# Kernel tuning notes

Hardware: AMD Instinct MI355X
Metric: run time of the kernel (lower is better)

The kernel has to match this reference:

```python
import jax, jax.numpy as jnp
import numpy as np

B, OBS, ACT_DIM, C, CTX, H = 128, 512, 7, 100, 128, 512
IN = OBS + 1 + CTX  # states + scalar action component + context = 641


def cont2disc(values, n):
    return jnp.clip(jnp.floor((values + 1.0) / 2.0 * n), 0, n - 1)


def setup_inputs() -> dict:
    key = jax.random.key(0)
    ks = jax.random.split(key, 10)
    def w(k, shape):
        return jax.random.normal(k, shape, dtype=jnp.float32) / np.sqrt(shape[-2])
    return {
        "observations": jax.random.normal(ks[0], (B, OBS), dtype=jnp.float32),
        "actions": jax.random.uniform(ks[1], (B, ACT_DIM), dtype=jnp.float32, minval=-1.0, maxval=1.0),
        # one MLP per action dim (weight_sharing=False): layers IN->H->H->CTX
        "W1": w(ks[2], (ACT_DIM, IN, H)),  "b1": jnp.zeros((ACT_DIM, H), jnp.float32),
        "W2": w(ks[3], (ACT_DIM, H, H)),   "b2": jnp.zeros((ACT_DIM, H), jnp.float32),
        "W3": w(ks[4], (ACT_DIM, H, CTX)), "b3": jnp.zeros((ACT_DIM, CTX), jnp.float32),
        # output_proj = MLP((1,)): single dense CTX->1, no activation
        "Wp": w(ks[5], (CTX, 1)), "bp": jnp.zeros((1,), jnp.float32),
        "compute_lse": 1,
    }


def reference(observations, actions, W1, b1, W2, b2, W3, b3, Wp, bp, compute_lse):
    n = observations.shape[0]
    acts = cont2disc(actions, C)  # [B, ACT_DIM], float component indices
    context = jnp.zeros((n, CTX), observations.dtype)
    comp = jnp.arange(C, dtype=observations.dtype)  # candidate components 0..C-1
    q = jnp.zeros((n, ACT_DIM * C), observations.dtype)

    for i in range(1, ACT_DIM):
        def mlp(x, i=i):  # hidden layers relu, final layer linear
            h = jax.nn.relu(x @ W1[i] + b1[i])
            h = jax.nn.relu(h @ W2[i] + b2[i])
            return h @ W3[i] + b3[i]

        # batched over all num_components candidate actions (replaces the per-j loop)
        xin = jnp.concatenate([
            jnp.broadcast_to(observations[:, None, :], (n, C, OBS)),
            jnp.broadcast_to(comp[None, :, None], (n, C, 1)),
            jnp.broadcast_to(context[:, None, :], (n, C, CTX)),
        ], axis=-1)  # [B, C, IN]
        curr_ctx = mlp(xin) + context[:, None, :]        # [B, C, CTX]
        qv = (curr_ctx @ Wp + bp)[..., 0]                # [B, C]
        q = q.at[:, (i - 1) * C : i * C].set(qv)          # which_qval ordering

        # advance context with the actual (discretized) action
        x = jnp.concatenate([observations, acts[:, i:i + 1], context], axis=-1)
        context = mlp(x) + context

    if compute_lse:
        return jax.scipy.special.logsumexp(q, axis=-1)    # [B]
    return context @ Wp + bp                              # [B, 1]
```

## Files before the change

### kernel.cpp

```cpp
#include <hip/hip_runtime.h>
#include <math.h>

#define BATCH 128
#define ACT 7
#define NC 100
#define CTXD 128
#define HID 512
#define QW 600

typedef __attribute__((ext_vector_type(8))) __bf16 bf16x8;
typedef __attribute__((ext_vector_type(4))) float f32x4;
typedef __attribute__((ext_vector_type(8))) unsigned short u16x8;
typedef __attribute__((ext_vector_type(4))) unsigned short u16x4;

__device__ __forceinline__ unsigned short f2bf(float f) {
    union { float f; unsigned int u; } v; v.f = f;
    unsigned int u = v.u;
    return (unsigned short)((u + 0x7fffu + ((u >> 16) & 1u)) >> 16);
}

__device__ __forceinline__ void async16(const void* g, void* l) {
    __builtin_amdgcn_global_load_lds(
        (const __attribute__((address_space(1))) unsigned int*)(uintptr_t)g,
        (__attribute__((address_space(3))) unsigned int*)(unsigned int)(uintptr_t)l,
        16, 0, 0);
}

__global__ void cvt_kernel(const float* __restrict__ obs, const float* __restrict__ W1,
                           const float* __restrict__ W2, const float* __restrict__ W3,
                           unsigned short* __restrict__ obs_bf, unsigned short* __restrict__ W1Cbf,
                           unsigned short* __restrict__ W2bf, unsigned short* __restrict__ W3bf) {
    const int e = (blockIdx.x * 256 + threadIdx.x) * 4;
    const float* src; unsigned short* dst;
    if (e < 65536)        { src = obs + e; dst = obs_bf + e; }
    else if (e < 458752)  { int f = e - 65536; int i = f >> 16; int rem = f & 65535;
                            src = W1 + (size_t)(i + 1) * 328192 + 513*512 + rem; dst = W1Cbf + f; }
    else if (e < 2031616) { int f = e - 458752; src = W2 + 262144 + f; dst = W2bf + f; }
    else                  { int f = e - 2031616; src = W3 + 65536 + f; dst = W3bf + f; }
    float4 v = *(const float4*)src;
    u16x4 o; o[0] = f2bf(v.x); o[1] = f2bf(v.y); o[2] = f2bf(v.z); o[3] = f2bf(v.w);
    *(u16x4*)dst = o;
}

__global__ void prep_transpose(const float* __restrict__ W1, const float* __restrict__ W2,
                               const float* __restrict__ W3,
                               unsigned short* __restrict__ W1AT, unsigned short* __restrict__ W2T,
                               unsigned short* __restrict__ W3T) {
    __shared__ float tile[32][33];
    const int z = blockIdx.z;
    const float* ip; unsigned short* op; int Cn;
    if (z < 6)       { ip = W1 + (size_t)(z + 1) * 328192; op = W1AT + (size_t)z * 262144; Cn = 512; }
    else if (z < 12) { int i = z - 6;  ip = W2 + (size_t)(i + 1) * 262144; op = W2T + (size_t)i * 262144; Cn = 512; }
    else             { int i = z - 12; ip = W3 + (size_t)(i + 1) * 65536;  op = W3T + (size_t)i * 65536;  Cn = 128;
                       if (blockIdx.y >= 4) return; }
    const int r0 = blockIdx.x * 32, c0 = blockIdx.y * 32;
    const int tx = threadIdx.x, ty = threadIdx.y;
    #pragma unroll
    for (int j = 0; j < 32; j += 8)
        tile[ty + j][tx] = ip[(size_t)(r0 + ty + j) * Cn + c0 + tx];
    __syncthreads();
    #pragma unroll
    for (int j = 0; j < 32; j += 8)
        op[(size_t)(c0 + ty + j) * 512 + r0 + tx] = f2bf(tile[tx][ty + j]);
}

__launch_bounds__(256)
__global__ void yobs_kernel(const unsigned short* __restrict__ A,
                            const unsigned short* __restrict__ BtAll,
                            const float* __restrict__ b1,
                            float* __restrict__ Yobs) {
    __shared__ unsigned short As[64*32];
    __shared__ unsigned short Bs[128*32];
    const int m0 = blockIdx.x * 64;
    const int n0 = blockIdx.y * 128;
    const int z  = blockIdx.z;
    const unsigned short* Bt = BtAll + (size_t)z * 262144;
    const int tid = threadIdx.x, lane = tid & 63, wave = tid >> 6;
    const int wm = wave >> 1, wn = wave & 1;
    const int srow = tid >> 2, skc = (tid & 3) * 8;
    const unsigned short* gA  = A  + (size_t)(m0 + srow) * HID + skc;
    const unsigned short* gB0 = Bt + (size_t)(n0 + srow) * HID + skc;
    const unsigned short* gB1 = gB0 + 64 * HID;
    f32x4 acc[2][4] = {};
    for (int k0 = 0; k0 < HID; k0 += 32) {
        async16(gA + k0, As + tid*8);
        async16(gB0 + k0, Bs + tid*8);
        async16(gB1 + k0, Bs + 2048 + tid*8);
        __syncthreads();
        const int q8 = (lane >> 4) * 8, l15 = lane & 15;
        bf16x8 af[2], bfr[4];
        #pragma unroll
        for (int mt = 0; mt < 2; ++mt)
            af[mt] = *(const bf16x8*)(As + (wm*32 + mt*16 + l15) * 32 + q8);
        #pragma unroll
        for (int nt = 0; nt < 4; ++nt)
            bfr[nt] = *(const bf16x8*)(Bs + (wn*64 + nt*16 + l15) * 32 + q8);
        #pragma unroll
        for (int mt = 0; mt < 2; ++mt)
            #pragma unroll
            for (int nt = 0; nt < 4; ++nt)
                acc[mt][nt] = __builtin_amdgcn_mfma_f32_16x16x32_bf16(af[mt], bfr[nt], acc[mt][nt], 0, 0, 0);
        __syncthreads();
    }
    const int colL = wn*64 + (lane & 15);
    #pragma unroll
    for (int nt = 0; nt < 4; ++nt) {
        const int col = n0 + colL + nt*16;
        const float bb = b1[(z + 1) * HID + col];
        #pragma unroll
        for (int mt = 0; mt < 2; ++mt)
            #pragma unroll
            for (int r = 0; r < 4; ++r) {
                const int row = m0 + wm*32 + mt*16 + (lane >> 4)*4 + r;
                Yobs[(size_t)z * 65536 + (size_t)row * HID + col] = acc[mt][nt][r] + bb;
            }
    }
}

__launch_bounds__(1024)
__global__ void chain_kernel(const float* __restrict__ Yobs, const float* __restrict__ W1,
                             const unsigned short* __restrict__ W1Cbf,
                             const unsigned short* __restrict__ W2bf,
                             const unsigned short* __restrict__ W3bf,
                             const float* __restrict__ b2, const float* __restrict__ b3,
                             const float* __restrict__ actions,
                             float* __restrict__ Y0all, float* __restrict__ CTXS) {
    const int b = blockIdx.x, t = threadIdx.x;
    __shared__ float ctx[128], h1[512], h2s[512];
    __shared__ float part[2048];
    const int pair = t & 255, kq = t >> 8;
    const int pair3 = t & 63, kq3 = t >> 6;
    if (t < 128) ctx[t] = 0.f;
    __syncthreads();
    for (int i = 1; i <= 6; ++i) {
        if (t < 128) CTXS[(size_t)(i-1)*16384 + b*128 + t] = ctx[t];
        const float a = actions[b*ACT + i];
        float fj = floorf((a + 1.0f) * 50.0f);
        fj = fminf(fmaxf(fj, 0.0f), 99.0f);
        {
            const unsigned int* wp1 = (const unsigned int*)(W1Cbf + (size_t)(i-1)*65536) + pair;
            float acc0 = 0.f, acc1 = 0.f;
            #pragma unroll 8
            for (int k = kq*32; k < kq*32 + 32; ++k) {
                unsigned int u = wp1[k*256];
                float c = ctx[k];
                acc0 = fmaf(c, __uint_as_float(u << 16), acc0);
                acc1 = fmaf(c, __uint_as_float(u & 0xffff0000u), acc1);
            }
            *(float2*)(&part[kq*512 + 2*pair]) = make_float2(acc0, acc1);
        }
        __syncthreads();
        if (t < 256) {
            const int n2 = 2*t;
            float2 p0 = *(const float2*)(&part[n2]);
            float2 p1 = *(const float2*)(&part[512 + n2]);
            float2 p2 = *(const float2*)(&part[1024 + n2]);
            float2 p3 = *(const float2*)(&part[1536 + n2]);
            float2 yo = *(const float2*)(Yobs + (size_t)(i-1)*65536 + b*512 + n2);
            float y0a = yo.x + p0.x + p1.x + p2.x + p3.x;
            float y0b = yo.y + p0.y + p1.y + p2.y + p3.y;
            *(float2*)(Y0all + (size_t)(i-1)*65536 + b*512 + n2) = make_float2(y0a, y0b);
            const float* w1a = W1 + (size_t)i*328192 + 262144;
            float2 wv = *(const float2*)(w1a + n2);
            h1[n2]   = fmaxf(fmaf(fj, wv.x, y0a), 0.f);
            h1[n2+1] = fmaxf(fmaf(fj, wv.y, y0b), 0.f);
        }
        __syncthreads();
        {
            const unsigned int* wp2 = (const unsigned int*)(W2bf + (size_t)(i-1)*262144) + pair;
            float acc0 = 0.f, acc1 = 0.f;
            #pragma unroll 8
            for (int k = kq*128; k < kq*128 + 128; ++k) {
                unsigned int u = wp2[k*256];
                float hv = h1[k];
                acc0 = fmaf(hv, __uint_as_float(u << 16), acc0);
                acc1 = fmaf(hv, __uint_as_float(u & 0xffff0000u), acc1);
            }
            *(float2*)(&part[kq*512 + 2*pair]) = make_float2(acc0, acc1);
        }
        __syncthreads();
        if (t < 256) {
            const int n2 = 2*t;
            float2 p0 = *(const float2*)(&part[n2]);
            float2 p1 = *(const float2*)(&part[512 + n2]);
            float2 p2 = *(const float2*)(&part[1024 + n2]);
            float2 p3 = *(const float2*)(&part[1536 + n2]);
            float2 bb = *(const float2*)(b2 + i*512 + n2);
            h2s[n2]   = fmaxf(p0.x + p1.x + p2.x + p3.x + bb.x, 0.f);
            h2s[n2+1] = fmaxf(p0.y + p1.y + p2.y + p3.y + bb.y, 0.f);
        }
        __syncthreads();
        {
            const unsigned int* wp3 = (const unsigned int*)(W3bf + (size_t)(i-1)*65536) + pair3;
            float acc0 = 0.f, acc1 = 0.f;
            #pragma unroll 8
            for (int k = kq3*32; k < kq3*32 + 32; ++k) {
                unsigned int u = wp3[k*64];
                float hv = h2s[k];
                acc0 = fmaf(hv, __uint_as_float(u << 16), acc0);
                acc1 = fmaf(hv, __uint_as_float(u & 0xffff0000u), acc1);
            }
            *(float2*)(&part[kq3*128 + 2*pair3]) = make_float2(acc0, acc1);
        }
        __syncthreads();
        if (t < 128) {
            float s = 0.f;
            #pragma unroll
            for (int qg = 0; qg < 16; ++qg) s += part[qg*128 + t];
            ctx[t] = s + b3[i*128 + t] + ctx[t];
        }
        __syncthreads();
    }
}

__launch_bounds__(256)
__global__ void h2all_kernel(const float* __restrict__ Y0all, const float* __restrict__ W1,
                             const unsigned short* __restrict__ W2T, const float* __restrict__ b2,
                             unsigned short* __restrict__ H2) {
    __shared__ unsigned short As[2][4096];
    __shared__ unsigned short Bs[2][4096];
    const int bx = blockIdx.x;
    const int z  = bx / 100;
    const int r0 = bx * 128;
    const int r2 = (bx % 100) * 128;
    const int n0 = blockIdx.y * 128;
    const int tid = threadIdx.x, lane = tid & 63, wave = tid >> 6;
    const int wm = wave >> 1, wn = wave & 1;
    const int srow = tid >> 2, skc = (tid & 3) * 8;
    const int l15 = lane & 15, q8 = (lane >> 4) * 8;
    const int rA = srow, kc = skc;
    const int rowg1 = r2 + rA, rowg2 = r2 + rA + 64;
    const float c1 = (float)(rowg1 % 100), c2 = (float)(rowg2 % 100);
    const float* y1p = Y0all + (size_t)z*65536 + (size_t)(rowg1/100)*512;
    const float* y2p = Y0all + (size_t)z*65536 + (size_t)(rowg2/100)*512;
    const float* w1a = W1 + (size_t)(z+1)*328192 + 262144;
    const unsigned short* gB0 = W2T + (size_t)z*262144 + (size_t)(n0 + srow)*512 + skc;
    const unsigned short* gB1 = gB0 + 64*512;
    f32x4 acc[4][4] = {};
    for (int k0 = 0; k0 < 512; k0 += 64) {
        #pragma unroll
        for (int h = 0; h < 2; ++h) {
            const int k = k0 + h*32 + kc;
            float4 wv0 = *(const float4*)(w1a + k);
            float4 wv1 = *(const float4*)(w1a + k + 4);
            float4 ya0 = *(const float4*)(y1p + k);
            float4 ya1 = *(const float4*)(y1p + k + 4);
            float4 yb0 = *(const float4*)(y2p + k);
            float4 yb1 = *(const float4*)(y2p + k + 4);
            u16x8 o1, o2;
            o1[0] = f2bf(fmaxf(fmaf(c1, wv0.x, ya0.x), 0.f));
            o1[1] = f2bf(fmaxf(fmaf(c1, wv0.y, ya0.y), 0.f));
            o1[2] = f2bf(fmaxf(fmaf(c1, wv0.z, ya0.z), 0.f));
            o1[3] = f2bf(fmaxf(fmaf(c1, wv0.w, ya0.w), 0.f));
            o1[4] = f2bf(fmaxf(fmaf(c1, wv1.x, ya1.x), 0.f));
            o1[5] = f2bf(fmaxf(fmaf(c1, wv1.y, ya1.y), 0.f));
            o1[6] = f2bf(fmaxf(fmaf(c1, wv1.z, ya1.z), 0.f));
            o1[7] = f2bf(fmaxf(fmaf(c1, wv1.w, ya1.w), 0.f));
            o2[0] = f2bf(fmaxf(fmaf(c2, wv0.x, yb0.x), 0.f));
            o2[1] = f2bf(fmaxf(fmaf(c2, wv0.y, yb0.y), 0.f));
            o2[2] = f2bf(fmaxf(fmaf(c2, wv0.z, yb0.z), 0.f));
            o2[3] = f2bf(fmaxf(fmaf(c2, wv0.w, yb0.w), 0.f));
            o2[4] = f2bf(fmaxf(fmaf(c2, wv1.x, yb1.x), 0.f));
            o2[5] = f2bf(fmaxf(fmaf(c2, wv1.y, yb1.y), 0.f));
            o2[6] = f2bf(fmaxf(fmaf(c2, wv1.z, yb1.z), 0.f));
            o2[7] = f2bf(fmaxf(fmaf(c2, wv1.w, yb1.w), 0.f));
            *(u16x8*)(&As[h][rA*32 + kc]) = o1;
            *(u16x8*)(&As[h][(rA + 64)*32 + kc]) = o2;
        }
        async16(gB0 + k0,      &Bs[0][tid*8]);
        async16(gB1 + k0,      &Bs[0][2048 + tid*8]);
        async16(gB0 + k0 + 32, &Bs[1][tid*8]);
        async16(gB1 + k0 + 32, &Bs[1][2048 + tid*8]);
        __syncthreads();
        #pragma unroll
        for (int h = 0; h < 2; ++h) {
            bf16x8 af[4], bfr[4];
            #pragma unroll
            for (int mt = 0; mt < 4; ++mt)
                af[mt] = *(const bf16x8*)(&As[h][(wm*64 + mt*16 + l15)*32 + q8]);
            #pragma unroll
            for (int nt = 0; nt < 4; ++nt)
                bfr[nt] = *(const bf16x8*)(&Bs[h][(wn*64 + nt*16 + l15)*32 + q8]);
            #pragma unroll
            for (int mt = 0; mt < 4; ++mt)
                #pragma unroll
                for (int nt = 0; nt < 4; ++nt)
                    acc[mt][nt] = __builtin_amdgcn_mfma_f32_16x16x32_bf16(af[mt], bfr[nt], acc[mt][nt], 0, 0, 0);
        }
        __syncthreads();
    }
    #pragma unroll
    for (int nt = 0; nt < 4; ++nt) {
        const int col = n0 + wn*64 + nt*16 + l15;
        const float bb = b2[(z+1)*512 + col];
        #pragma unroll
        for (int mt = 0; mt < 4; ++mt)
            #pragma unroll
            for (int r = 0; r < 4; ++r) {
                const int row = r0 + wm*64 + mt*16 + (lane >> 4)*4 + r;
                H2[(size_t)row * 512 + col] = f2bf(fmaxf(acc[mt][nt][r] + bb, 0.f));
            }
    }
}

__launch_bounds__(256)
__global__ void gemm3all_kernel(const unsigned short* __restrict__ H2,
                                const unsigned short* __restrict__ W3T,
                                const float* __restrict__ b3, const float* __restrict__ CTXS,
                                const float* __restrict__ Wp, const float* __restrict__ bp,
                                float* __restrict__ q) {
    __shared__ unsigned short As[2][1024];
    __shared__ unsigned short Bs[2][4096];
    __shared__ float CCs[32][132];
    __shared__ float qp[32][8];
    const int bx = blockIdx.x;
    const int z  = bx / 400;
    const int r0 = bx * 32;
    const int r2 = (bx % 400) * 32;
    const int tid = threadIdx.x, lane = tid & 63, wave = tid >> 6;
    const int wm = wave >> 1, wn = wave & 1;
    const int srow = tid >> 2, skc = (tid & 3) * 8;
    const int l15 = lane & 15, q8 = (lane >> 4) * 8;
    const unsigned short* gB0 = W3T + (size_t)z*65536 + (size_t)srow*512 + skc;
    const unsigned short* gB1 = gB0 + 64*512;
    const unsigned short* gA  = H2 + (size_t)(r0 + srow)*512 + skc;
    f32x4 acc[4] = {};
    for (int k0 = 0; k0 < 512; k0 += 64) {
        if (tid < 128) {
            async16(gA + k0,      &As[0][tid*8]);
            async16(gA + k0 + 32, &As[1][tid*8]);
        }
        async16(gB0 + k0,      &Bs[0][tid*8]);
        async16(gB1 + k0,      &Bs[0][2048 + tid*8]);
        async16(gB0 + k0 + 32, &Bs[1][tid*8]);
        async16(gB1 + k0 + 32, &Bs[1][2048 + tid*8]);
        __syncthreads();
        #pragma unroll
        for (int h = 0; h < 2; ++h) {
            bf16x8 af = *(const bf16x8*)(&As[h][(wm*16 + l15)*32 + q8]);
            #pragma unroll
            for (int nt = 0; nt < 4; ++nt) {
                bf16x8 bfr = *(const bf16x8*)(&Bs[h][(wn*64 + nt*16 + l15)*32 + q8]);
                acc[nt] = __builtin_amdgcn_mfma_f32_16x16x32_bf16(af, bfr, acc[nt], 0, 0, 0);
            }
        }
        __syncthreads();
    }
    #pragma unroll
    for (int nt = 0; nt < 4; ++nt) {
        const int col = wn*64 + nt*16 + l15;
        const float bb = b3[(z+1)*128 + col];
        #pragma unroll
        for (int r = 0; r < 4; ++r) {
            const int rowL = wm*16 + (lane >> 4)*4 + r;
            const int gb = (r2 + rowL) / 100;
            CCs[rowL][col] = acc[nt][r] + bb + CTXS[(size_t)z*16384 + gb*128 + col];
        }
    }
    __syncthreads();
    {
        const int rowL = tid >> 3, seg = tid & 7;
        float s = 0.f;
        #pragma unroll
        for (int j = 0; j < 16; ++j) s += CCs[rowL][seg*16 + j] * Wp[seg*16 + j];
        qp[rowL][seg] = s;
    }
    __syncthreads();
    if (tid < 32) {
        const int gr2 = r2 + tid;
        const int gb = gr2 / 100, gc = gr2 - gb * 100;
        float s = qp[tid][0] + qp[tid][1] + qp[tid][2] + qp[tid][3]
                + qp[tid][4] + qp[tid][5] + qp[tid][6] + qp[tid][7];
        q[gb * QW + z * 100 + gc] = s + bp[0];
    }
}

__global__ void lse_kernel(const float* __restrict__ q, float* __restrict__ out) {
    __shared__ float red[256];
    int b = blockIdx.x, t = threadIdx.x;
    float m = 0.0f;
    for (int k = t; k < QW; k += 256) m = fmaxf(m, q[b*QW + k]);
    red[t] = m; __syncthreads();
    for (int s = 128; s > 0; s >>= 1) { if (t < s) red[t] = fmaxf(red[t], red[t+s]); __syncthreads(); }
    m = red[0]; __syncthreads();
    float sum = 0.0f;
    for (int k = t; k < QW; k += 256) sum += expf(q[b*QW + k] - m);
    red[t] = sum; __syncthreads();
    for (int s = 128; s > 0; s >>= 1) { if (t < s) red[t] += red[t+s]; __syncthreads(); }
    if (t == 0) out[b] = logf(red[0] + 100.0f * expf(-m)) + m;
}

extern "C" void kernel_launch(void* const* d_in, const int* in_sizes, int n_in,
                              void* d_out, int out_size, void* d_ws, size_t ws_size,
                              hipStream_t stream) {
    const float* obs     = (const float*)d_in[0];
    const float* actions = (const float*)d_in[1];
    const float* W1      = (const float*)d_in[2];
    const float* b1      = (const float*)d_in[3];
    const float* W2      = (const float*)d_in[4];
    const float* b2      = (const float*)d_in[5];
    const float* W3      = (const float*)d_in[6];
    const float* b3      = (const float*)d_in[7];
    const float* Wp      = (const float*)d_in[8];
    const float* bp      = (const float*)d_in[9];
    float* out = (float*)d_out;
    float* ws  = (float*)d_ws;

    unsigned short* obs_bf = (unsigned short*)(ws);
    unsigned short* W1AT   = (unsigned short*)(ws + 32768);
    unsigned short* W2T    = (unsigned short*)(ws + 819200);
    unsigned short* W3T    = (unsigned short*)(ws + 1605632);
    unsigned short* W1Cbf  = (unsigned short*)(ws + 1802240);
    unsigned short* W2bf   = (unsigned short*)(ws + 1998848);
    unsigned short* W3bf   = (unsigned short*)(ws + 2785280);
    float* Yobs  = ws + 2981888;
    float* Y0all = ws + 3375104;
    float* CTXS  = ws + 3768320;
    float* q     = ws + 3866624;
    unsigned short* H2 = (unsigned short*)(ws + 3943424);

    cvt_kernel<<<2368, 256, 0, stream>>>(obs, W1, W2, W3, obs_bf, W1Cbf, W2bf, W3bf);
    prep_transpose<<<dim3(16,16,18), dim3(32,8), 0, stream>>>(W1, W2, W3, W1AT, W2T, W3T);
    yobs_kernel<<<dim3(2,4,6), 256, 0, stream>>>(obs_bf, W1AT, b1, Yobs);
    chain_kernel<<<BATCH, 1024, 0, stream>>>(Yobs, W1, W1Cbf, W2bf, W3bf, b2, b3, actions, Y0all, CTXS);
    h2all_kernel<<<dim3(600, 4), 256, 0, stream>>>(Y0all, W1, W2T, b2, H2);
    gemm3all_kernel<<<2400, 256, 0, stream>>>(H2, W3T, b3, CTXS, Wp, bp, q);
    lse_kernel<<<BATCH, 256, 0, stream>>>(q, out);
}
```

Before: 263.3 us.

## Retile layer-2 and layer-3 GEMMs to full-width N with 64-row blocks

The h2all GEMM now gives each block 64 rows and all 512 output columns, with a 32-wide K step. The fused ReLU/first-layer A tile is therefore computed once per row instead of once per 128-column slice, which removes the fourfold recomputation and the repeated Y0all reads. gemm3all moves from 32-row to 64-row tiles so each W3 tile load is reused across more rows, and the chain kernel's layer-2 loop gets a larger unroll. In exchange the per-thread accumulator count grows to 32 f32x4 vectors, which raises register pressure (launch bounds now ask for two blocks per CU). The K loop also does twice as many barrier steps with no double buffering.

Measured after the change: 269.4 us. 2.3% more time.

```diff
diff --git a/kernel.cpp b/kernel.cpp
--- a/kernel.cpp
+++ b/kernel.cpp
@@ -169,7 +169,7 @@
         {
             const unsigned int* wp2 = (const unsigned int*)(W2bf + (size_t)(i-1)*262144) + pair;
             float acc0 = 0.f, acc1 = 0.f;
-            #pragma unroll 8
+            #pragma unroll 16
             for (int k = kq*128; k < kq*128 + 128; ++k) {
                 unsigned int u = wp2[k*256];
                 float hv = h1[k];
@@ -213,91 +213,72 @@
     }
 }
 
-__launch_bounds__(256)
+__launch_bounds__(256, 2)
 __global__ void h2all_kernel(const float* __restrict__ Y0all, const float* __restrict__ W1,
                              const unsigned short* __restrict__ W2T, const float* __restrict__ b2,
                              unsigned short* __restrict__ H2) {
-    __shared__ unsigned short As[2][4096];
-    __shared__ unsigned short Bs[2][4096];
+    __shared__ unsigned short ASl[64*32];
+    __shared__ unsigned short BSl[512*32];
     const int bx = blockIdx.x;
-    const int z  = bx / 100;
-    const int r0 = bx * 128;
-    const int r2 = (bx % 100) * 128;
-    const int n0 = blockIdx.y * 128;
+    const int z  = bx / 200;
+    const int r0 = bx * 64;
+    const int r2 = (bx % 200) * 64;
     const int tid = threadIdx.x, lane = tid & 63, wave = tid >> 6;
-    const int wm = wave >> 1, wn = wave & 1;
-    const int srow = tid >> 2, skc = (tid & 3) * 8;
     const int l15 = lane & 15, q8 = (lane >> 4) * 8;
-    const int rA = srow, kc = skc;
-    const int rowg1 = r2 + rA, rowg2 = r2 + rA + 64;
-    const float c1 = (float)(rowg1 % 100), c2 = (float)(rowg2 % 100);
-    const float* y1p = Y0all + (size_t)z*65536 + (size_t)(rowg1/100)*512;
-    const float* y2p = Y0all + (size_t)z*65536 + (size_t)(rowg2/100)*512;
-    const float* w1a = W1 + (size_t)(z+1)*328192 + 262144;
-    const unsigned short* gB0 = W2T + (size_t)z*262144 + (size_t)(n0 + srow)*512 + skc;
-    const unsigned short* gB1 = gB0 + 64*512;
-    f32x4 acc[4][4] = {};
-    for (int k0 = 0; k0 < 512; k0 += 64) {
-        #pragma unroll
-        for (int h = 0; h < 2; ++h) {
-            const int k = k0 + h*32 + kc;
-            float4 wv0 = *(const float4*)(w1a + k);
-            float4 wv1 = *(const float4*)(w1a + k + 4);
-            float4 ya0 = *(const float4*)(y1p + k);
-            float4 ya1 = *(const float4*)(y1p + k + 4);
-            float4 yb0 = *(const float4*)(y2p + k);
-            float4 yb1 = *(const float4*)(y2p + k + 4);
-            u16x8 o1, o2;
-            o1[0] = f2bf(fmaxf(fmaf(c1, wv0.x, ya0.x), 0.f));
-            o1[1] = f2bf(fmaxf(fmaf(c1, wv0.y, ya0.y), 0.f));
-            o1[2] = f2bf(fmaxf(fmaf(c1, wv0.z, ya0.z), 0.f));
-            o1[3] = f2bf(fmaxf(fmaf(c1, wv0.w, ya0.w), 0.f));
-            o1[4] = f2bf(fmaxf(fmaf(c1, wv1.x, ya1.x), 0.f));
-            o1[5] = f2bf(fmaxf(fmaf(c1, wv1.y, ya1.y), 0.f));
-            o1[6] = f2bf(fmaxf(fmaf(c1, wv1.z, ya1.z), 0.f));
-            o1[7] = f2bf(fmaxf(fmaf(c1, wv1.w, ya1.w), 0.f));
-            o2[0] = f2bf(fmaxf(fmaf(c2, wv0.x, yb0.x), 0.f));
-            o2[1] = f2bf(fmaxf(fmaf(c2, wv0.y, yb0.y), 0.f));
-            o2[2] = f2bf(fmaxf(fmaf(c2, wv0.z, yb0.z), 0.f));
-            o2[3] = f2bf(fmaxf(fmaf(c2, wv0.w, yb0.w), 0.f));
-            o2[4] = f2bf(fmaxf(fmaf(c2, wv1.x, yb1.x), 0.f));
-            o2[5] = f2bf(fmaxf(fmaf(c2, wv1.y, yb1.y), 0.f));
-            o2[6] = f2bf(fmaxf(fmaf(c2, wv1.z, yb1.z), 0.f));
-            o2[7] = f2bf(fmaxf(fmaf(c2, wv1.w, yb1.w), 0.f));
-            *(u16x8*)(&As[h][rA*32 + kc]) = o1;
-            *(u16x8*)(&As[h][(rA + 64)*32 + kc]) = o2;
-        }
-        async16(gB0 + k0,      &Bs[0][tid*8]);
-        async16(gB1 + k0,      &Bs[0][2048 + tid*8]);
-        async16(gB0 + k0 + 32, &Bs[1][tid*8]);
-        async16(gB1 + k0 + 32, &Bs[1][2048 + tid*8]);
-        __syncthreads();
-        #pragma unroll
-        for (int h = 0; h < 2; ++h) {
-            bf16x8 af[4], bfr[4];
-            #pragma unroll
-            for (int mt = 0; mt < 4; ++mt)
-                af[mt] = *(const bf16x8*)(&As[h][(wm*64 + mt*16 + l15)*32 + q8]);
-            #pragma unroll
-            for (int nt = 0; nt < 4; ++nt)
-                bfr[nt] = *(const bf16x8*)(&Bs[h][(wn*64 + nt*16 + l15)*32 + q8]);
-            #pragma unroll
-            for (int mt = 0; mt < 4; ++mt)
-                #pragma unroll
-                for (int nt = 0; nt < 4; ++nt)
-                    acc[mt][nt] = __builtin_amdgcn_mfma_f32_16x16x32_bf16(af[mt], bfr[nt], acc[mt][nt], 0, 0, 0);
-        }
+    const int rA = tid >> 2, kc8 = (tid & 3) * 8;
+    const int growA = r2 + rA;
+    const float cA = (float)(growA % 100);
+    const float* yp  = Y0all + (size_t)z*65536 + (size_t)(growA/100)*512 + kc8;
+    const float* w1a = W1 + (size_t)(z+1)*328192 + 262144 + kc8;
+    const unsigned short* W2Tz = W2T + (size_t)z*262144;
+    f32x4 acc[4][8] = {};
+    for (int k0 = 0; k0 < 512; k0 += 32) {
+        {
+            float4 y0v = *(const float4*)(yp + k0);
+            float4 y1v = *(const float4*)(yp + k0 + 4);
+            float4 w0v = *(const float4*)(w1a + k0);
+            float4 w1v = *(const float4*)(w1a + k0 + 4);
+            u16x8 o;
+            o[0] = f2bf(fmaxf(fmaf(cA, w0v.x, y0v.x), 0.f));
+            o[1] = f2bf(fmaxf(fmaf(cA, w0v.y, y0v.y), 0.f));
+            o[2] = f2bf(fmaxf(fmaf(cA, w0v.z, y0v.z), 0.f));
+            o[3] = f2bf(fmaxf(fmaf(cA, w0v.w, y0v.w), 0.f));
+            o[4] = f2bf(fmaxf(fmaf(cA, w1v.x, y1v.x), 0.f));
+            o[5] = f2bf(fmaxf(fmaf(cA, w1v.y, y1v.y), 0.f));
+            o[6] = f2bf(fmaxf(fmaf(cA, w1v.z, y1v.z), 0.f));
+            o[7] = f2bf(fmaxf(fmaf(cA, w1v.w, y1v.w), 0.f));
+            *(u16x8*)(ASl + rA*32 + kc8) = o;
+        }
+        #pragma unroll
+        for (int c = 0; c < 8; ++c) {
+            const int s = c*256 + wave*64 + lane;
+            const int col = s >> 2, sub = s & 3;
+            async16(W2Tz + (size_t)col*512 + k0 + sub*8, BSl + (size_t)s*8);
+        }
+        __syncthreads();
+        bf16x8 af[4], bfr[8];
+        #pragma unroll
+        for (int mt = 0; mt < 4; ++mt)
+            af[mt] = *(const bf16x8*)(ASl + (mt*16 + l15)*32 + q8);
+        #pragma unroll
+        for (int nt = 0; nt < 8; ++nt)
+            bfr[nt] = *(const bf16x8*)(BSl + (wave*128 + nt*16 + l15)*32 + q8);
+        #pragma unroll
+        for (int mt = 0; mt < 4; ++mt)
+            #pragma unroll
+            for (int nt = 0; nt < 8; ++nt)
+                acc[mt][nt] = __builtin_amdgcn_mfma_f32_16x16x32_bf16(af[mt], bfr[nt], acc[mt][nt], 0, 0, 0);
         __syncthreads();
     }
     #pragma unroll
-    for (int nt = 0; nt < 4; ++nt) {
-        const int col = n0 + wn*64 + nt*16 + l15;
+    for (int nt = 0; nt < 8; ++nt) {
+        const int col = wave*128 + nt*16 + l15;
         const float bb = b2[(z+1)*512 + col];
         #pragma unroll
         for (int mt = 0; mt < 4; ++mt)
             #pragma unroll
             for (int r = 0; r < 4; ++r) {
-                const int row = r0 + wm*64 + mt*16 + (lane >> 4)*4 + r;
+                const int row = r0 + mt*16 + (lane >> 4)*4 + r;
                 H2[(size_t)row * 512 + col] = f2bf(fmaxf(acc[mt][nt][r] + bb, 0.f));
             }
     }
@@ -309,41 +290,42 @@
                                 const float* __restrict__ b3, const float* __restrict__ CTXS,
                                 const float* __restrict__ Wp, const float* __restrict__ bp,
                                 float* __restrict__ q) {
-    __shared__ unsigned short As[2][1024];
-    __shared__ unsigned short Bs[2][4096];
-    __shared__ float CCs[32][132];
-    __shared__ float qp[32][8];
+    __shared__ unsigned short ASl[64*32];
+    __shared__ unsigned short BSl[128*32];
+    __shared__ float CCs[64][132];
+    __shared__ float qp[64][4];
     const int bx = blockIdx.x;
-    const int z  = bx / 400;
-    const int r0 = bx * 32;
-    const int r2 = (bx % 400) * 32;
+    const int z  = bx / 200;
+    const int r0 = bx * 64;
+    const int r2 = (bx % 200) * 64;
     const int tid = threadIdx.x, lane = tid & 63, wave = tid >> 6;
     const int wm = wave >> 1, wn = wave & 1;
-    const int srow = tid >> 2, skc = (tid & 3) * 8;
     const int l15 = lane & 15, q8 = (lane >> 4) * 8;
-    const unsigned short* gB0 = W3T + (size_t)z*65536 + (size_t)srow*512 + skc;
-    const unsigned short* gB1 = gB0 + 64*512;
-    const unsigned short* gA  = H2 + (size_t)(r0 + srow)*512 + skc;
-    f32x4 acc[4] = {};
-    for (int k0 = 0; k0 < 512; k0 += 64) {
-        if (tid < 128) {
-            async16(gA + k0,      &As[0][tid*8]);
-            async16(gA + k0 + 32, &As[1][tid*8]);
-        }
-        async16(gB0 + k0,      &Bs[0][tid*8]);
-        async16(gB1 + k0,      &Bs[0][2048 + tid*8]);
-        async16(gB0 + k0 + 32, &Bs[1][tid*8]);
-        async16(gB1 + k0 + 32, &Bs[1][2048 + tid*8]);
-        __syncthreads();
-        #pragma unroll
-        for (int h = 0; h < 2; ++h) {
-            bf16x8 af = *(const bf16x8*)(&As[h][(wm*16 + l15)*32 + q8]);
-            #pragma unroll
-            for (int nt = 0; nt < 4; ++nt) {
-                bf16x8 bfr = *(const bf16x8*)(&Bs[h][(wn*64 + nt*16 + l15)*32 + q8]);
-                acc[nt] = __builtin_amdgcn_mfma_f32_16x16x32_bf16(af, bfr, acc[nt], 0, 0, 0);
-            }
-        }
+    const unsigned short* W3Tz = W3T + (size_t)z*65536;
+    f32x4 acc[2][4] = {};
+    for (int k0 = 0; k0 < 512; k0 += 32) {
+        {
+            const int s = wave*64 + lane, row = s >> 2, sub = s & 3;
+            async16(H2 + (size_t)(r0 + row)*512 + k0 + sub*8, ASl + (size_t)s*8);
+        }
+        #pragma unroll
+        for (int c = 0; c < 2; ++c) {
+            const int s = c*256 + wave*64 + lane, col = s >> 2, sub = s & 3;
+            async16(W3Tz + (size_t)col*512 + k0 + sub*8, BSl + (size_t)s*8);
+        }
+        __syncthreads();
+        bf16x8 af[2], bfr[4];
+        #pragma unroll
+        for (int mt = 0; mt < 2; ++mt)
+            af[mt] = *(const bf16x8*)(ASl + (wm*32 + mt*16 + l15)*32 + q8);
+        #pragma unroll
+        for (int nt = 0; nt < 4; ++nt)
+            bfr[nt] = *(const bf16x8*)(BSl + (wn*64 + nt*16 + l15)*32 + q8);
+        #pragma unroll
+        for (int mt = 0; mt < 2; ++mt)
+            #pragma unroll
+            for (int nt = 0; nt < 4; ++nt)
+                acc[mt][nt] = __builtin_amdgcn_mfma_f32_16x16x32_bf16(af[mt], bfr[nt], acc[mt][nt], 0, 0, 0);
         __syncthreads();
     }
     #pragma unroll
@@ -351,26 +333,27 @@
         const int col = wn*64 + nt*16 + l15;
         const float bb = b3[(z+1)*128 + col];
         #pragma unroll
-        for (int r = 0; r < 4; ++r) {
-            const int rowL = wm*16 + (lane >> 4)*4 + r;
-            const int gb = (r2 + rowL) / 100;
-            CCs[rowL][col] = acc[nt][r] + bb + CTXS[(size_t)z*16384 + gb*128 + col];
-        }
+        for (int mt = 0; mt < 2; ++mt)
+            #pragma unroll
+            for (int r = 0; r < 4; ++r) {
+                const int rowL = wm*32 + mt*16 + (lane >> 4)*4 + r;
+                const int gb = (r2 + rowL) / 100;
+                CCs[rowL][col] = acc[mt][nt][r] + bb + CTXS[(size_t)z*16384 + gb*128 + col];
+            }
     }
     __syncthreads();
     {
-        const int rowL = tid >> 3, seg = tid & 7;
+        const int rowL = tid >> 2, seg = tid & 3;
         float s = 0.f;
         #pragma unroll
-        for (int j = 0; j < 16; ++j) s += CCs[rowL][seg*16 + j] * Wp[seg*16 + j];
+        for (int j = 0; j < 32; ++j) s += CCs[rowL][seg*32 + j] * Wp[seg*32 + j];
         qp[rowL][seg] = s;
     }
     __syncthreads();
-    if (tid < 32) {
+    if (tid < 64) {
         const int gr2 = r2 + tid;
         const int gb = gr2 / 100, gc = gr2 - gb * 100;
-        float s = qp[tid][0] + qp[tid][1] + qp[tid][2] + qp[tid][3]
-                + qp[tid][4] + qp[tid][5] + qp[tid][6] + qp[tid][7];
+        float s = qp[tid][0] + qp[tid][1] + qp[tid][2] + qp[tid][3];
         q[gb * QW + z * 100 + gc] = s + bp[0];
     }
 }
@@ -423,7 +406,7 @@
     prep_transpose<<<dim3(16,16,18), dim3(32,8), 0, stream>>>(W1, W2, W3, W1AT, W2T, W3T);
     yobs_kernel<<<dim3(2,4,6), 256, 0, stream>>>(obs_bf, W1AT, b1, Yobs);
     chain_kernel<<<BATCH, 1024, 0, stream>>>(Yobs, W1, W1Cbf, W2bf, W3bf, b2, b3, actions, Y0all, CTXS);
-    h2all_kernel<<<dim3(600, 4), 256, 0, stream>>>(Y0all, W1, W2T, b2, H2);
-    gemm3all_kernel<<<2400, 256, 0, stream>>>(H2, W3T, b3, CTXS, Wp, bp, q);
+    h2all_kernel<<<1200, 256, 0, stream>>>(Y0all, W1, W2T, b2, H2);
+    gemm3all_kernel<<<1200, 256, 0, stream>>>(H2, W3T, b3, CTXS, Wp, bp, q);
     lse_kernel<<<BATCH, 256, 0, stream>>>(q, out);
 }
```

## Fold W3 and output projection into a vector, fuse into layer-2 GEMM epilogue

Applied to the files above, without the earlier changes.

Because the last MLP layer and the output projection are both linear, W3 times Wp is precomputed as one 512-vector per action dim. The layer-2 GEMM epilogue then computes the q contribution directly as a dot product of relu(h2) with that vector. Context and bias terms become a per-batch offset computed in the chain kernel. This removes the bf16 H2 intermediate, the W3 transpose and the whole third GEMM kernel, and adds a small partial-sum reduction in lse. It also switches to a cheaper packed bf16 rounding and raises one unroll factor.

Result: faster. 243.4 us (-7.6%).

```diff
diff --git a/kernel.cpp b/kernel.cpp
--- a/kernel.cpp
+++ b/kernel.cpp
@@ -10,13 +10,17 @@
 
 typedef __attribute__((ext_vector_type(8))) __bf16 bf16x8;
 typedef __attribute__((ext_vector_type(4))) float f32x4;
-typedef __attribute__((ext_vector_type(8))) unsigned short u16x8;
 typedef __attribute__((ext_vector_type(4))) unsigned short u16x4;
 
 __device__ __forceinline__ unsigned short f2bf(float f) {
     union { float f; unsigned int u; } v; v.f = f;
     unsigned int u = v.u;
     return (unsigned short)((u + 0x7fffu + ((u >> 16) & 1u)) >> 16);
+}
+__device__ __forceinline__ unsigned int pack2bf(float a, float b) {
+    unsigned int ua = __float_as_uint(a) + 0x8000u;
+    unsigned int ub = __float_as_uint(b) + 0x8000u;
+    return (ua >> 16) | (ub & 0xffff0000u);
 }
 
 __device__ __forceinline__ void async16(const void* g, void* l) {
@@ -43,25 +47,35 @@
 }
 
 __global__ void prep_transpose(const float* __restrict__ W1, const float* __restrict__ W2,
-                               const float* __restrict__ W3,
-                               unsigned short* __restrict__ W1AT, unsigned short* __restrict__ W2T,
-                               unsigned short* __restrict__ W3T) {
+                               unsigned short* __restrict__ W1AT, unsigned short* __restrict__ W2T) {
     __shared__ float tile[32][33];
     const int z = blockIdx.z;
-    const float* ip; unsigned short* op; int Cn;
-    if (z < 6)       { ip = W1 + (size_t)(z + 1) * 328192; op = W1AT + (size_t)z * 262144; Cn = 512; }
-    else if (z < 12) { int i = z - 6;  ip = W2 + (size_t)(i + 1) * 262144; op = W2T + (size_t)i * 262144; Cn = 512; }
-    else             { int i = z - 12; ip = W3 + (size_t)(i + 1) * 65536;  op = W3T + (size_t)i * 65536;  Cn = 128;
-                       if (blockIdx.y >= 4) return; }
+    const float* ip; unsigned short* op;
+    if (z < 6) { ip = W1 + (size_t)(z + 1) * 328192; op = W1AT + (size_t)z * 262144; }
+    else       { int i = z - 6; ip = W2 + (size_t)(i + 1) * 262144; op = W2T + (size_t)i * 262144; }
     const int r0 = blockIdx.x * 32, c0 = blockIdx.y * 32;
     const int tx = threadIdx.x, ty = threadIdx.y;
     #pragma unroll
     for (int j = 0; j < 32; j += 8)
-        tile[ty + j][tx] = ip[(size_t)(r0 + ty + j) * Cn + c0 + tx];
+        tile[ty + j][tx] = ip[(size_t)(r0 + ty + j) * 512 + c0 + tx];
     __syncthreads();
     #pragma unroll
     for (int j = 0; j < 32; j += 8)
         op[(size_t)(c0 + ty + j) * 512 + r0 + tx] = f2bf(tile[tx][ty + j]);
+}
+
+__global__ void vq_kernel(const float* __restrict__ W3, const float* __restrict__ Wp,
+                          float* __restrict__ vq) {
+    const int z = blockIdx.x, k = threadIdx.x;
+    const float4* row = (const float4*)(W3 + (size_t)(z + 1) * 65536 + (size_t)k * 128);
+    const float4* wp4 = (const float4*)Wp;
+    float s = 0.f;
+    #pragma unroll 8
+    for (int n = 0; n < 32; ++n) {
+        float4 a = row[n], w = wp4[n];
+        s += a.x*w.x + a.y*w.y + a.z*w.z + a.w*w.w;
+    }
+    vq[z * 512 + k] = s;
 }
 
 __launch_bounds__(256)
@@ -124,7 +138,8 @@
                              const unsigned short* __restrict__ W3bf,
                              const float* __restrict__ b2, const float* __restrict__ b3,
                              const float* __restrict__ actions,
-                             float* __restrict__ Y0all, float* __restrict__ CTXS) {
+                             const float* __restrict__ Wp, const float* __restrict__ bp,
+                             float* __restrict__ Y0all, float* __restrict__ QOFF) {
     const int b = blockIdx.x, t = threadIdx.x;
     __shared__ float ctx[128], h1[512], h2s[512];
     __shared__ float part[2048];
@@ -133,7 +148,15 @@
     if (t < 128) ctx[t] = 0.f;
     __syncthreads();
     for (int i = 1; i <= 6; ++i) {
-        if (t < 128) CTXS[(size_t)(i-1)*16384 + b*128 + t] = ctx[t];
+        if (t < 128) part[t] = (ctx[t] + b3[i*128 + t]) * Wp[t];
+        __syncthreads();
+        if (t < 64) {
+            float v = part[t] + part[t + 64];
+            #pragma unroll
+            for (int o = 32; o > 0; o >>= 1) v += __shfl_down(v, o, 64);
+            if (t == 0) QOFF[(i-1)*128 + b] = v + bp[0];
+        }
+        __syncthreads();
         const float a = actions[b*ACT + i];
         float fj = floorf((a + 1.0f) * 50.0f);
         fj = fminf(fmaxf(fj, 0.0f), 99.0f);
@@ -169,7 +192,7 @@
         {
             const unsigned int* wp2 = (const unsigned int*)(W2bf + (size_t)(i-1)*262144) + pair;
             float acc0 = 0.f, acc1 = 0.f;
-            #pragma unroll 8
+            #pragma unroll 16
             for (int k = kq*128; k < kq*128 + 128; ++k) {
                 unsigned int u = wp2[k*256];
                 float hv = h1[k];
@@ -216,7 +239,7 @@
 __launch_bounds__(256)
 __global__ void h2all_kernel(const float* __restrict__ Y0all, const float* __restrict__ W1,
                              const unsigned short* __restrict__ W2T, const float* __restrict__ b2,
-                             unsigned short* __restrict__ H2) {
+                             const float* __restrict__ vq, float* __restrict__ qpart) {
     __shared__ unsigned short As[2][4096];
     __shared__ unsigned short Bs[2][4096];
     const int bx = blockIdx.x;
@@ -247,25 +270,17 @@
             float4 ya1 = *(const float4*)(y1p + k + 4);
             float4 yb0 = *(const float4*)(y2p + k);
             float4 yb1 = *(const float4*)(y2p + k + 4);
-            u16x8 o1, o2;
-            o1[0] = f2bf(fmaxf(fmaf(c1, wv0.x, ya0.x), 0.f));
-            o1[1] = f2bf(fmaxf(fmaf(c1, wv0.y, ya0.y), 0.f));
-            o1[2] = f2bf(fmaxf(fmaf(c1, wv0.z, ya0.z), 0.f));
-            o1[3] = f2bf(fmaxf(fmaf(c1, wv0.w, ya0.w), 0.f));
-            o1[4] = f2bf(fmaxf(fmaf(c1, wv1.x, ya1.x), 0.f));
-            o1[5] = f2bf(fmaxf(fmaf(c1, wv1.y, ya1.y), 0.f));
-            o1[6] = f2bf(fmaxf(fmaf(c1, wv1.z, ya1.z), 0.f));
-            o1[7] = f2bf(fmaxf(fmaf(c1, wv1.w, ya1.w), 0.f));
-            o2[0] = f2bf(fmaxf(fmaf(c2, wv0.x, yb0.x), 0.f));
-            o2[1] = f2bf(fmaxf(fmaf(c2, wv0.y, yb0.y), 0.f));
-            o2[2] = f2bf(fmaxf(fmaf(c2, wv0.z, yb0.z), 0.f));
-            o2[3] = f2bf(fmaxf(fmaf(c2, wv0.w, yb0.w), 0.f));
-            o2[4] = f2bf(fmaxf(fmaf(c2, wv1.x, yb1.x), 0.f));
-            o2[5] = f2bf(fmaxf(fmaf(c2, wv1.y, yb1.y), 0.f));
-            o2[6] = f2bf(fmaxf(fmaf(c2, wv1.z, yb1.z), 0.f));
-            o2[7] = f2bf(fmaxf(fmaf(c2, wv1.w, yb1.w), 0.f));
-            *(u16x8*)(&As[h][rA*32 + kc]) = o1;
-            *(u16x8*)(&As[h][(rA + 64)*32 + kc]) = o2;
+            uint4 o;
+            o.x = pack2bf(fmaxf(fmaf(c1, wv0.x, ya0.x), 0.f), fmaxf(fmaf(c1, wv0.y, ya0.y), 0.f));
+            o.y = pack2bf(fmaxf(fmaf(c1, wv0.z, ya0.z), 0.f), fmaxf(fmaf(c1, wv0.w, ya0.w), 0.f));
+            o.z = pack2bf(fmaxf(fmaf(c1, wv1.x, ya1.x), 0.f), fmaxf(fmaf(c1, wv1.y, ya1.y), 0.f));
+            o.w = pack2bf(fmaxf(fmaf(c1, wv1.z, ya1.z), 0.f), fmaxf(fmaf(c1, wv1.w, ya1.w), 0.f));
+            *(uint4*)(&As[h][rA*32 + kc]) = o;
+            o.x = pack2bf(fmaxf(fmaf(c2, wv0.x, yb0.x), 0.f), fmaxf(fmaf(c2, wv0.y, yb0.y), 0.f));
+            o.y = pack2bf(fmaxf(fmaf(c2, wv0.z, yb0.z), 0.f), fmaxf(fmaf(c2, wv0.w, yb0.w), 0.f));
+            o.z = pack2bf(fmaxf(fmaf(c2, wv1.x, yb1.x), 0.f), fmaxf(fmaf(c2, wv1.y, yb1.y), 0.f));
+            o.w = pack2bf(fmaxf(fmaf(c2, wv1.z, yb1.z), 0.f), fmaxf(fmaf(c2, wv1.w, yb1.w), 0.f));
+            *(uint4*)(&As[h][(rA + 64)*32 + kc]) = o;
         }
         async16(gB0 + k0,      &Bs[0][tid*8]);
         async16(gB1 + k0,      &Bs[0][2048 + tid*8]);
@@ -289,102 +304,55 @@
         }
         __syncthreads();
     }
+    float vb[4], bb[4];
     #pragma unroll
     for (int nt = 0; nt < 4; ++nt) {
         const int col = n0 + wn*64 + nt*16 + l15;
-        const float bb = b2[(z+1)*512 + col];
-        #pragma unroll
-        for (int mt = 0; mt < 4; ++mt)
-            #pragma unroll
-            for (int r = 0; r < 4; ++r) {
-                const int row = r0 + wm*64 + mt*16 + (lane >> 4)*4 + r;
-                H2[(size_t)row * 512 + col] = f2bf(fmaxf(acc[mt][nt][r] + bb, 0.f));
-            }
-    }
-}
-
-__launch_bounds__(256)
-__global__ void gemm3all_kernel(const unsigned short* __restrict__ H2,
-                                const unsigned short* __restrict__ W3T,
-                                const float* __restrict__ b3, const float* __restrict__ CTXS,
-                                const float* __restrict__ Wp, const float* __restrict__ bp,
-                                float* __restrict__ q) {
-    __shared__ unsigned short As[2][1024];
-    __shared__ unsigned short Bs[2][4096];
-    __shared__ float CCs[32][132];
-    __shared__ float qp[32][8];
-    const int bx = blockIdx.x;
-    const int z  = bx / 400;
-    const int r0 = bx * 32;
-    const int r2 = (bx % 400) * 32;
-    const int tid = threadIdx.x, lane = tid & 63, wave = tid >> 6;
-    const int wm = wave >> 1, wn = wave & 1;
-    const int srow = tid >> 2, skc = (tid & 3) * 8;
-    const int l15 = lane & 15, q8 = (lane >> 4) * 8;
-    const unsigned short* gB0 = W3T + (size_t)z*65536 + (size_t)srow*512 + skc;
-    const unsigned short* gB1 = gB0 + 64*512;
-    const unsigned short* gA  = H2 + (size_t)(r0 + srow)*512 + skc;
-    f32x4 acc[4] = {};
-    for (int k0 = 0; k0 < 512; k0 += 64) {
-        if (tid < 128) {
-            async16(gA + k0,      &As[0][tid*8]);
-            async16(gA + k0 + 32, &As[1][tid*8]);
-        }
-        async16(gB0 + k0,      &Bs[0][tid*8]);
-        async16(gB1 + k0,      &Bs[0][2048 + tid*8]);
-        async16(gB0 + k0 + 32, &Bs[1][tid*8]);
-        async16(gB1 + k0 + 32, &Bs[1][2048 + tid*8]);
-        __syncthreads();
-        #pragma unroll
-        for (int h = 0; h < 2; ++h) {
-            bf16x8 af = *(const bf16x8*)(&As[h][(wm*16 + l15)*32 + q8]);
-            #pragma unroll
-            for (int nt = 0; nt < 4; ++nt) {
-                bf16x8 bfr = *(const bf16x8*)(&Bs[h][(wn*64 + nt*16 + l15)*32 + q8]);
-                acc[nt] = __builtin_amdgcn_mfma_f32_16x16x32_bf16(af, bfr, acc[nt], 0, 0, 0);
-            }
-        }
-        __syncthreads();
-    }
-    #pragma unroll
-    for (int nt = 0; nt < 4; ++nt) {
-        const int col = wn*64 + nt*16 + l15;
-        const float bb = b3[(z+1)*128 + col];
+        bb[nt] = b2[(z+1)*512 + col];
+        vb[nt] = vq[z*512 + col];
+    }
+    const int plane = blockIdx.y * 2 + wn;
+    const int gq = lane >> 4;
+    #pragma unroll
+    for (int mt = 0; mt < 4; ++mt)
         #pragma unroll
         for (int r = 0; r < 4; ++r) {
-            const int rowL = wm*16 + (lane >> 4)*4 + r;
-            const int gb = (r2 + rowL) / 100;
-            CCs[rowL][col] = acc[nt][r] + bb + CTXS[(size_t)z*16384 + gb*128 + col];
-        }
+            float p = 0.f;
+            #pragma unroll
+            for (int nt = 0; nt < 4; ++nt)
+                p = fmaf(fmaxf(acc[mt][nt][r] + bb[nt], 0.f), vb[nt], p);
+            p += __shfl_xor(p, 1, 64);
+            p += __shfl_xor(p, 2, 64);
+            p += __shfl_xor(p, 4, 64);
+            p += __shfl_xor(p, 8, 64);
+            if (l15 == 0) {
+                const int grow = r0 + wm*64 + mt*16 + gq*4 + r;
+                qpart[(size_t)plane * 76800 + grow] = p;
+            }
+        }
+}
+
+__global__ void lse_kernel(const float* __restrict__ qpart, const float* __restrict__ QOFF,
+                           float* __restrict__ out) {
+    __shared__ float red[256];
+    __shared__ float qs[QW];
+    const int b = blockIdx.x, t = threadIdx.x;
+    for (int k = t; k < QW; k += 256) {
+        const int z = k / 100, gc = k - z * 100;
+        const int grow = z * 12800 + b * 100 + gc;
+        float s = QOFF[z * 128 + b];
+        #pragma unroll
+        for (int p = 0; p < 8; ++p) s += qpart[(size_t)p * 76800 + grow];
+        qs[k] = s;
     }
     __syncthreads();
-    {
-        const int rowL = tid >> 3, seg = tid & 7;
-        float s = 0.f;
-        #pragma unroll
-        for (int j = 0; j < 16; ++j) s += CCs[rowL][seg*16 + j] * Wp[seg*16 + j];
-        qp[rowL][seg] = s;
-    }
-    __syncthreads();
-    if (tid < 32) {
-        const int gr2 = r2 + tid;
-        const int gb = gr2 / 100, gc = gr2 - gb * 100;
-        float s = qp[tid][0] + qp[tid][1] + qp[tid][2] + qp[tid][3]
-                + qp[tid][4] + qp[tid][5] + qp[tid][6] + qp[tid][7];
-        q[gb * QW + z * 100 + gc] = s + bp[0];
-    }
-}
-
-__global__ void lse_kernel(const float* __restrict__ q, float* __restrict__ out) {
-    __shared__ float red[256];
-    int b = blockIdx.x, t = threadIdx.x;
     float m = 0.0f;
-    for (int k = t; k < QW; k += 256) m = fmaxf(m, q[b*QW + k]);
+    for (int k = t; k < QW; k += 256) m = fmaxf(m, qs[k]);
     red[t] = m; __syncthreads();
     for (int s = 128; s > 0; s >>= 1) { if (t < s) red[t] = fmaxf(red[t], red[t+s]); __syncthreads(); }
     m = red[0]; __syncthreads();
     float sum = 0.0f;
-    for (int k = t; k < QW; k += 256) sum += expf(q[b*QW + k] - m);
+    for (int k = t; k < QW; k += 256) sum += expf(qs[k] - m);
     red[t] = sum; __syncthreads();
     for (int s = 128; s > 0; s >>= 1) { if (t < s) red[t] += red[t+s]; __syncthreads(); }
     if (t == 0) out[b] = logf(red[0] + 100.0f * expf(-m)) + m;
@@ -409,21 +377,20 @@
     unsigned short* obs_bf = (unsigned short*)(ws);
     unsigned short* W1AT   = (unsigned short*)(ws + 32768);
     unsigned short* W2T    = (unsigned short*)(ws + 819200);
-    unsigned short* W3T    = (unsigned short*)(ws + 1605632);
-    unsigned short* W1Cbf  = (unsigned short*)(ws + 1802240);
-    unsigned short* W2bf   = (unsigned short*)(ws + 1998848);
-    unsigned short* W3bf   = (unsigned short*)(ws + 2785280);
-    float* Yobs  = ws + 2981888;
-    float* Y0all = ws + 3375104;
-    float* CTXS  = ws + 3768320;
-    float* q     = ws + 3866624;
-    unsigned short* H2 = (unsigned short*)(ws + 3943424);
+    unsigned short* W1Cbf  = (unsigned short*)(ws + 1605632);
+    unsigned short* W2bf   = (unsigned short*)(ws + 1802240);
+    unsigned short* W3bf   = (unsigned short*)(ws + 2588672);
+    float* Yobs  = ws + 2785280;
+    float* Y0all = ws + 3178496;
+    float* QOFF  = ws + 3571712;
+    float* vq    = ws + 3572736;
+    float* qpart = ws + 3575808;
 
     cvt_kernel<<<2368, 256, 0, stream>>>(obs, W1, W2, W3, obs_bf, W1Cbf, W2bf, W3bf);
-    prep_transpose<<<dim3(16,16,18), dim3(32,8), 0, stream>>>(W1, W2, W3, W1AT, W2T, W3T);
+    prep_transpose<<<dim3(16,16,12), dim3(32,8), 0, stream>>>(W1, W2, W1AT, W2T);
+    vq_kernel<<<6, 512, 0, stream>>>(W3, Wp, vq);
     yobs_kernel<<<dim3(2,4,6), 256, 0, stream>>>(obs_bf, W1AT, b1, Yobs);
-    chain_kernel<<<BATCH, 1024, 0, stream>>>(Yobs, W1, W1Cbf, W2bf, W3bf, b2, b3, actions, Y0all, CTXS);
-    h2all_kernel<<<dim3(600, 4), 256, 0, stream>>>(Y0all, W1, W2T, b2, H2);
-    gemm3all_kernel<<<2400, 256, 0, stream>>>(H2, W3T, b3, CTXS, Wp, bp, q);
-    lse_kernel<<<BATCH, 256, 0, stream>>>(q, out);
-}
+    chain_kernel<<<BATCH, 1024, 0, stream>>>(Yobs, W1, W1Cbf, W2bf, W3bf, b2, b3, actions, Wp, bp, Y0all, QOFF);
+    h2all_kernel<<<dim3(600, 4), 256, 0, stream>>>(Y0all, W1, W2T, b2, vq, qpart);
+    lse_kernel<<<BATCH, 256, 0, stream>>>(qpart, QOFF, out);
+}
```
